# Optimization experiments

Measured on AMD Instinct MI355X. Metric: run time of the kernel, lower is better.

Reference implementation:

```python
import jax, jax.numpy as jnp
import numpy as np


def postorder_positions(depth):
    """Post-order index of each node in a perfect binary tree of given depth.
    Returns dict: level -> np.array of post-order indices for the left-to-right
    nodes at that level (level 0 = leaves, level `depth` = root)."""
    levels = {0: np.array([0], dtype=np.int64)}
    size = 1  # size of depth-(d-1) subtree
    for d in range(1, depth + 1):
        new = {l: np.concatenate([levels[l], levels[l] + size]) for l in range(d)}
        new[d] = np.array([2 * size], dtype=np.int64)
        levels = new
        size = 2 * size + 1
    return levels


def setup_inputs() -> dict:
    key = jax.random.key(0)
    k1, k2, k3, k4, k5, k6 = jax.random.split(key, 6)
    VOCAB, E, LBL, LEAVES = 50000, 100, 2, 131072  # 2**17 leaves
    word_ids = jax.random.randint(k1, (LEAVES,), 0, VOCAB, dtype=jnp.int32)
    emb_table = jax.random.normal(k2, (VOCAB, E), dtype=jnp.float32) * 0.1
    Wl = jax.random.normal(k3, (E, E), dtype=jnp.float32) * 0.1
    bl = jax.random.normal(k4, (E,), dtype=jnp.float32) * 0.1
    Wp = jax.random.normal(k5, (LBL, E), dtype=jnp.float32) * 0.1
    bp = jax.random.normal(k6, (LBL,), dtype=jnp.float32) * 0.1
    return {"word_ids": word_ids, "emb_table": emb_table, "Wl": Wl, "bl": bl, "Wp": Wp, "bp": bp}


def reference(word_ids, emb_table, Wl, bl, Wp, bp):
    # Perfect binary tree, batched level-by-level (same math as the per-node
    # Python recursion in the torch module). NOTE: original uses fcl for BOTH
    # children, so internal node = relu(fcl(left) + fcl(right)).
    L = word_ids.shape[0]
    D = int(round(np.log2(L)))
    pos = postorder_positions(D)
    n_nodes = 2 * L - 1

    h = emb_table[word_ids]  # [L, E] leaf states
    out = jnp.zeros((n_nodes, 1, bp.shape[0]), dtype=h.dtype)
    for lvl in range(D + 1):
        proj = h @ Wp.T + bp                     # [n_lvl, label]
        out = out.at[jnp.asarray(pos[lvl])].set(proj[:, None, :])
        if lvl < D:
            # fcl(left)+fcl(right) = (left+right) @ Wl^T + 2*bl, then relu
            h = jax.nn.relu((h[0::2] + h[1::2]) @ Wl.T + 2.0 * bl)
    return out  # [n_nodes, 1, label] in post-order, matching torch.cat(node_list)
```

## Files before the change

kernel.cpp:

```cpp
#include <hip/hip_runtime.h>

typedef _Float16 h8v __attribute__((ext_vector_type(8)));
typedef float f4v __attribute__((ext_vector_type(4)));

#define RS 136
#define SD 68

__device__ __forceinline__ unsigned pk2f(float a, float b) {
  unsigned short ha = __builtin_bit_cast(unsigned short, (_Float16)a);
  unsigned short hb = __builtin_bit_cast(unsigned short, (_Float16)b);
  return (unsigned)ha | ((unsigned)hb << 16);
}
__device__ __forceinline__ float2 upk(unsigned u) {
  _Float16 lo = __builtin_bit_cast(_Float16, (unsigned short)(u & 0xffffu));
  _Float16 hi = __builtin_bit_cast(_Float16, (unsigned short)(u >> 16));
  return make_float2((float)lo, (float)hi);
}

__global__ void prep_kernel(const float* __restrict__ Wl,
                            unsigned short* __restrict__ Wlf) {
  int i = blockIdx.x * 256 + threadIdx.x;
  if (i < 128 * 128) {
    int o = i >> 7, k = i & 127;
    _Float16 v = (_Float16)0.f;
    if (o < 100 && k < 100) v = (_Float16)Wl[o * 100 + k];
    Wlf[i] = __builtin_bit_cast(unsigned short, v);
  }
}

__device__ __forceinline__ void load_bfrags(
    const unsigned short* __restrict__ Wlf, const float* __restrict__ bl,
    h8v (&B0)[4], h8v (&B1)[4], float& bias0, float& bias1,
    int wave, int quad, int c16) {
  int col0 = wave * 32 + c16;
  int col1 = col0 + 16;
  bias0 = (col0 < 100) ? 2.0f * bl[col0] : 0.f;
  bias1 = (col1 < 100) ? 2.0f * bl[col1] : 0.f;
  const _Float16* w0 = (const _Float16*)Wlf + col0 * 128 + quad * 8;
  const _Float16* w1 = (const _Float16*)Wlf + col1 * 128 + quad * 8;
  B0[0] = *(const h8v*)(w0);      B0[1] = *(const h8v*)(w0 + 32);
  B0[2] = *(const h8v*)(w0 + 64); B0[3] = *(const h8v*)(w0 + 96);
  B1[0] = *(const h8v*)(w1);      B1[1] = *(const h8v*)(w1 + 32);
  B1[2] = *(const h8v*)(w1 + 64); B1[3] = *(const h8v*)(w1 + 96);
}

__device__ __forceinline__ void mfma_level(
    const _Float16* srcE, const _Float16* srcO, bool pairMode,
    _Float16* dstE, _Float16* dstO, int nOut,
    const h8v (&B0)[4], const h8v (&B1)[4], float bias0, float bias1,
    int lane, int wave) {
  const int quad = lane >> 4, c16 = lane & 15;
  const int col0 = wave * 32 + c16, col1 = col0 + 16;
  const int tiles = (nOut + 15) >> 4;
  for (int rt = 0; rt < tiles; ++rt) {
    const int r = rt * 16 + c16;
    const h8v* pe = (const h8v*)(srcE + (size_t)r * RS + quad * 8);
    h8v A0, A1, A2, A3;
    if (pairMode) {
      const h8v* po = (const h8v*)(srcO + (size_t)r * RS + quad * 8);
      A0 = pe[0] + po[0];  A1 = pe[4] + po[4];
      A2 = pe[8] + po[8];  A3 = pe[12] + po[12];
    } else {
      A0 = pe[0]; A1 = pe[4]; A2 = pe[8]; A3 = pe[12];
    }
    f4v a0 = {bias0, bias0, bias0, bias0};
    f4v a1 = {bias1, bias1, bias1, bias1};
    a0 = __builtin_amdgcn_mfma_f32_16x16x32_f16(A0, B0[0], a0, 0, 0, 0);
    a0 = __builtin_amdgcn_mfma_f32_16x16x32_f16(A1, B0[1], a0, 0, 0, 0);
    a0 = __builtin_amdgcn_mfma_f32_16x16x32_f16(A2, B0[2], a0, 0, 0, 0);
    a0 = __builtin_amdgcn_mfma_f32_16x16x32_f16(A3, B0[3], a0, 0, 0, 0);
    a1 = __builtin_amdgcn_mfma_f32_16x16x32_f16(A0, B1[0], a1, 0, 0, 0);
    a1 = __builtin_amdgcn_mfma_f32_16x16x32_f16(A1, B1[1], a1, 0, 0, 0);
    a1 = __builtin_amdgcn_mfma_f32_16x16x32_f16(A2, B1[2], a1, 0, 0, 0);
    a1 = __builtin_amdgcn_mfma_f32_16x16x32_f16(A3, B1[3], a1, 0, 0, 0);
    #pragma unroll
    for (int rg = 0; rg < 4; ++rg) {
      int row = rt * 16 + quad * 4 + rg;
      _Float16* dr = ((row & 1) ? dstO : dstE) + (size_t)(row >> 1) * RS;
      dr[col0] = (_Float16)fmaxf(a0[rg], 0.f);
      dr[col1] = (_Float16)fmaxf(a1[rg], 0.f);
    }
  }
}

__device__ __forceinline__ void proj_rows(
    const _Float16* E, const _Float16* O, int nRows, const float* WpS,
    float bp0, float bp1, int lvl, long gbase, float* __restrict__ out, int tid) {
  if (tid >= nRows) return;
  const unsigned* row = (const unsigned*)((tid & 1) ? O : E) + (size_t)(tid >> 1) * SD;
  float q0 = bp0, q1 = bp1;
  #pragma unroll
  for (int p = 0; p < 25; ++p) {
    uint2 u = ((const uint2*)row)[p];
    float2 a = upk(u.x), b = upk(u.y);
    q0 = fmaf(a.x, WpS[4*p], fmaf(a.y, WpS[4*p+1],
         fmaf(b.x, WpS[4*p+2], fmaf(b.y, WpS[4*p+3], q0))));
    q1 = fmaf(a.x, WpS[100+4*p], fmaf(a.y, WpS[100+4*p+1],
         fmaf(b.x, WpS[100+4*p+2], fmaf(b.y, WpS[100+4*p+3], q1))));
  }
  long g = gbase + tid;
  long pos = ((g + 1) << (lvl + 1)) - 2 - __popc((unsigned)g);
  out[2 * pos] = q0; out[2 * pos + 1] = q1;
}

__global__ __launch_bounds__(256, 3) void leaf_kernel(
    const int* __restrict__ word_ids, const float* __restrict__ emb,
    const unsigned short* __restrict__ Wlf, const float* __restrict__ bl,
    const float* __restrict__ Wp, const float* __restrict__ bp,
    unsigned* __restrict__ h7g, float* __restrict__ out) {
  __shared__ _Float16 S1[64 * RS];
  __shared__ _Float16 Ea[32 * RS], Oa[32 * RS];
  __shared__ _Float16 Eb[16 * RS], Ob[16 * RS];
  __shared__ float WpS[200];
  const int tid = threadIdx.x, lane = tid & 63;
  const int wave = __builtin_amdgcn_readfirstlane(tid >> 6);
  const int quad = lane >> 4, c16 = lane & 15;
  const int blk = blockIdx.x;

  if (tid < 200) WpS[tid] = Wp[tid];
  {
    unsigned* S1d = (unsigned*)S1;
    for (int i = tid; i < 64 * 14; i += 256) S1d[(i / 14) * SD + 50 + (i % 14)] = 0;
  }
  const float bp0 = bp[0], bp1 = bp[1];

  const int l = tid >> 1, hh = tid & 1;
  const long gL = (long)blk * 128 + l;
  const float4* row4 = (const float4*)(emb + (size_t)word_ids[gL] * 100);
  float4 v[13];
  #pragma unroll
  for (int i = 0; i < 13; ++i) {
    int q = 13 * hh + i;
    if (q < 25) v[i] = row4[q];
  }
  __syncthreads();

  {
    float q0 = 0.f, q1 = 0.f;
    #pragma unroll
    for (int i = 0; i < 13; ++i) {
      int q = 13 * hh + i;
      if (q < 25) {
        q0 = fmaf(v[i].x, WpS[4*q], fmaf(v[i].y, WpS[4*q+1],
             fmaf(v[i].z, WpS[4*q+2], fmaf(v[i].w, WpS[4*q+3], q0))));
        q1 = fmaf(v[i].x, WpS[100+4*q], fmaf(v[i].y, WpS[100+4*q+1],
             fmaf(v[i].z, WpS[100+4*q+2], fmaf(v[i].w, WpS[100+4*q+3], q1))));
      }
    }
    q0 += __shfl_xor(q0, 1, 64);
    q1 += __shfl_xor(q1, 1, 64);
    if (hh == 0) {
      long pos = ((gL + 1) << 1) - 2 - __popc((unsigned)gL);
      out[2 * pos] = q0 + bp0; out[2 * pos + 1] = q1 + bp1;
    }
  }
  {
    unsigned* S1d = (unsigned*)S1;
    #pragma unroll
    for (int i = 0; i < 13; ++i) {
      int q = 13 * hh + i;
      if (q < 25) {
        float sx = v[i].x + __shfl_xor(v[i].x, 2, 64);
        float sy = v[i].y + __shfl_xor(v[i].y, 2, 64);
        float sz = v[i].z + __shfl_xor(v[i].z, 2, 64);
        float sw = v[i].w + __shfl_xor(v[i].w, 2, 64);
        if ((tid & 2) == 0) {
          int m = tid >> 2;
          S1d[m * SD + 2*q]     = pk2f(sx, sy);
          S1d[m * SD + 2*q + 1] = pk2f(sz, sw);
        }
      }
    }
  }
  h8v B0[4], B1[4]; float bias0, bias1;
  load_bfrags(Wlf, bl, B0, B1, bias0, bias1, wave, quad, c16);
  __syncthreads();

  mfma_level(S1, nullptr, false, Ea, Oa, 64, B0, B1, bias0, bias1, lane, wave);
  __syncthreads();
  mfma_level(Ea, Oa, true, Eb, Ob, 32, B0, B1, bias0, bias1, lane, wave);
  proj_rows(Ea, Oa, 64, WpS, bp0, bp1, 1, (long)blk * 64, out, tid);
  __syncthreads();
  mfma_level(Eb, Ob, true, Ea, Oa, 16, B0, B1, bias0, bias1, lane, wave);
  proj_rows(Eb, Ob, 32, WpS, bp0, bp1, 2, (long)blk * 32, out, tid);
  __syncthreads();
  mfma_level(Ea, Oa, true, Eb, Ob, 8, B0, B1, bias0, bias1, lane, wave);
  proj_rows(Ea, Oa, 16, WpS, bp0, bp1, 3, (long)blk * 16, out, tid);
  __syncthreads();
  mfma_level(Eb, Ob, true, Ea, Oa, 4, B0, B1, bias0, bias1, lane, wave);
  proj_rows(Eb, Ob, 8, WpS, bp0, bp1, 4, (long)blk * 8, out, tid);
  __syncthreads();
  mfma_level(Ea, Oa, true, Eb, Ob, 2, B0, B1, bias0, bias1, lane, wave);
  proj_rows(Ea, Oa, 4, WpS, bp0, bp1, 5, (long)blk * 4, out, tid);
  __syncthreads();
  mfma_level(Eb, Ob, true, Ea, Oa, 1, B0, B1, bias0, bias1, lane, wave);
  proj_rows(Eb, Ob, 2, WpS, bp0, bp1, 6, (long)blk * 2, out, tid);
  __syncthreads();
  if (tid < 50) h7g[(size_t)blk * 50 + tid] = ((unsigned*)Ea)[tid];
}

__global__ __launch_bounds__(256) void tree_kernel(
    const unsigned* __restrict__ hsrc, unsigned* __restrict__ hdst,
    const unsigned short* __restrict__ Wlf, const float* __restrict__ bl,
    const float* __restrict__ Wp, const float* __restrict__ bp,
    float* __restrict__ out, int firstLvl, int nLvl, int nIn, int finalProj) {
  __shared__ _Float16 Ea[32 * RS], Oa[32 * RS];
  __shared__ _Float16 Eb[16 * RS], Ob[16 * RS];
  __shared__ float WpS[200];
  const int tid = threadIdx.x, lane = tid & 63;
  const int wave = __builtin_amdgcn_readfirstlane(tid >> 6);
  const int quad = lane >> 4, c16 = lane & 15;
  const int blk = blockIdx.x;

  if (tid < 200) WpS[tid] = Wp[tid];
  const float bp0 = bp[0], bp1 = bp[1];

  {
    const unsigned* src = hsrc + (size_t)blk * nIn * 50;
    unsigned* Ed = (unsigned*)Ea; unsigned* Od = (unsigned*)Oa;
    for (int i = tid; i < 64 * 64; i += 256) {
      int r = i >> 6, d = i & 63;
      unsigned val = (r < nIn && d < 50) ? src[(size_t)r * 50 + d] : 0u;
      ((r & 1) ? Od : Ed)[(r >> 1) * SD + d] = val;
    }
    unsigned* Ed2 = (unsigned*)Eb; unsigned* Od2 = (unsigned*)Ob;
    for (int i = tid; i < 32 * 64; i += 256) {
      int r = i >> 6, d = i & 63;
      ((r & 1) ? Od2 : Ed2)[(r >> 1) * SD + d] = 0u;
    }
  }
  h8v B0[4], B1[4]; float bias0, bias1;
  load_bfrags(Wlf, bl, B0, B1, bias0, bias1, wave, quad, c16);
  __syncthreads();

  _Float16 *sE = Ea, *sO = Oa, *dE = Eb, *dO = Ob;
  int n = nIn >> 1;
  for (int p = 0; p < nLvl; ++p) {
    mfma_level(sE, sO, true, dE, dO, n, B0, B1, bias0, bias1, lane, wave);
    proj_rows(sE, sO, n * 2, WpS, bp0, bp1, firstLvl + p - 1,
              (long)blk * (n * 2), out, tid);
    __syncthreads();
    _Float16* t;
    t = sE; sE = dE; dE = t;
    t = sO; sO = dO; dO = t;
    n >>= 1;
  }
  int R = nIn >> nLvl;
  if (finalProj)
    proj_rows(sE, sO, R, WpS, bp0, bp1, firstLvl + nLvl - 1, (long)blk * R, out, tid);
  if (hdst) {
    for (int i = tid; i < R * 50; i += 256) {
      int r = i / 50, d = i % 50;
      hdst[(size_t)blk * R * 50 + i] =
          ((const unsigned*)((r & 1) ? sO : sE))[(r >> 1) * SD + d];
    }
  }
}

extern "C" void kernel_launch(void* const* d_in, const int* in_sizes, int n_in,
                              void* d_out, int out_size, void* d_ws, size_t ws_size,
                              hipStream_t stream) {
  const int*   word_ids = (const int*)  d_in[0];
  const float* emb      = (const float*)d_in[1];
  const float* Wl       = (const float*)d_in[2];
  const float* bl       = (const float*)d_in[3];
  const float* Wp       = (const float*)d_in[4];
  const float* bp       = (const float*)d_in[5];
  float* out = (float*)d_out;

  unsigned short* Wlf = (unsigned short*)d_ws;
  unsigned* h7g  = (unsigned*)((char*)d_ws + 32768);
  unsigned* h13g = (unsigned*)((char*)d_ws + 32768 + 204800);

  prep_kernel<<<64, 256, 0, stream>>>(Wl, Wlf);
  leaf_kernel<<<1024, 256, 0, stream>>>(word_ids, emb, Wlf, bl, Wp, bp, h7g, out);
  tree_kernel<<<16, 256, 0, stream>>>(h7g, h13g, Wlf, bl, Wp, bp, out, 8, 6, 64, 0);
  tree_kernel<<<1, 256, 0, stream>>>(h13g, nullptr, Wlf, bl, Wp, bp, out, 14, 4, 16, 1);
}
```

Measured before the change: 152.2 us.

## Restructure tree into 512-thread leaf kernel and single tail kernel

The leaf kernel now runs 512 threads per block over 256 leaves, with waves split into column pairs and row halves, and reduces 8 levels in shared memory. The two small tree_kernel launches are replaced by one 512-thread tail kernel that reads the level-8 states from global memory and reduces the remaining levels. The aim is to cut a kernel launch and its serial dependency, and to use more waves on the tiny upper levels. The cost is larger shared memory per block (about 70KB for leaf, 100KB for tail), which lowers occupancy, and a single-block tail that serializes 9 levels.

Measured after the change: 152.3 us. About the same (+0.1%).

```diff
diff --git a/kernel.cpp b/kernel.cpp
--- a/kernel.cpp
+++ b/kernel.cpp
@@ -31,8 +31,8 @@
 __device__ __forceinline__ void load_bfrags(
     const unsigned short* __restrict__ Wlf, const float* __restrict__ bl,
     h8v (&B0)[4], h8v (&B1)[4], float& bias0, float& bias1,
-    int wave, int quad, int c16) {
-  int col0 = wave * 32 + c16;
+    int cp, int quad, int c16) {
+  int col0 = cp * 32 + c16;
   int col1 = col0 + 16;
   bias0 = (col0 < 100) ? 2.0f * bl[col0] : 0.f;
   bias1 = (col1 < 100) ? 2.0f * bl[col1] : 0.f;
@@ -44,15 +44,42 @@
   B1[2] = *(const h8v*)(w1 + 64); B1[3] = *(const h8v*)(w1 + 96);
 }
 
+__device__ __forceinline__ void mfma_8(
+    const h8v& A0, const h8v& A1, const h8v& A2, const h8v& A3,
+    const h8v (&B0)[4], const h8v (&B1)[4], float bias0, float bias1,
+    f4v& a0, f4v& a1) {
+  a0 = {bias0, bias0, bias0, bias0};
+  a1 = {bias1, bias1, bias1, bias1};
+  a0 = __builtin_amdgcn_mfma_f32_16x16x32_f16(A0, B0[0], a0, 0, 0, 0);
+  a0 = __builtin_amdgcn_mfma_f32_16x16x32_f16(A1, B0[1], a0, 0, 0, 0);
+  a0 = __builtin_amdgcn_mfma_f32_16x16x32_f16(A2, B0[2], a0, 0, 0, 0);
+  a0 = __builtin_amdgcn_mfma_f32_16x16x32_f16(A3, B0[3], a0, 0, 0, 0);
+  a1 = __builtin_amdgcn_mfma_f32_16x16x32_f16(A0, B1[0], a1, 0, 0, 0);
+  a1 = __builtin_amdgcn_mfma_f32_16x16x32_f16(A1, B1[1], a1, 0, 0, 0);
+  a1 = __builtin_amdgcn_mfma_f32_16x16x32_f16(A2, B1[2], a1, 0, 0, 0);
+  a1 = __builtin_amdgcn_mfma_f32_16x16x32_f16(A3, B1[3], a1, 0, 0, 0);
+}
+
+__device__ __forceinline__ void store_cd(
+    _Float16* dstE, _Float16* dstO, int rb, const f4v& a0, const f4v& a1,
+    int quad, int c16, int col0, int col1) {
+  #pragma unroll
+  for (int rg = 0; rg < 4; ++rg) {
+    int row = rb + quad * 4 + rg;
+    _Float16* dr = ((row & 1) ? dstO : dstE) + (size_t)(row >> 1) * RS;
+    dr[col0] = (_Float16)fmaxf(a0[rg], 0.f);
+    dr[col1] = (_Float16)fmaxf(a1[rg], 0.f);
+  }
+}
+
 __device__ __forceinline__ void mfma_level(
     const _Float16* srcE, const _Float16* srcO, bool pairMode,
     _Float16* dstE, _Float16* dstO, int nOut,
     const h8v (&B0)[4], const h8v (&B1)[4], float bias0, float bias1,
-    int lane, int wave) {
-  const int quad = lane >> 4, c16 = lane & 15;
-  const int col0 = wave * 32 + c16, col1 = col0 + 16;
+    int cp, int rowhalf, int quad, int c16) {
+  const int col0 = cp * 32 + c16, col1 = col0 + 16;
   const int tiles = (nOut + 15) >> 4;
-  for (int rt = 0; rt < tiles; ++rt) {
+  for (int rt = rowhalf; rt < tiles; rt += 2) {
     const int r = rt * 16 + c16;
     const h8v* pe = (const h8v*)(srcE + (size_t)r * RS + quad * 8);
     h8v A0, A1, A2, A3;
@@ -63,23 +90,28 @@
     } else {
       A0 = pe[0]; A1 = pe[4]; A2 = pe[8]; A3 = pe[12];
     }
-    f4v a0 = {bias0, bias0, bias0, bias0};
-    f4v a1 = {bias1, bias1, bias1, bias1};
-    a0 = __builtin_amdgcn_mfma_f32_16x16x32_f16(A0, B0[0], a0, 0, 0, 0);
-    a0 = __builtin_amdgcn_mfma_f32_16x16x32_f16(A1, B0[1], a0, 0, 0, 0);
-    a0 = __builtin_amdgcn_mfma_f32_16x16x32_f16(A2, B0[2], a0, 0, 0, 0);
-    a0 = __builtin_amdgcn_mfma_f32_16x16x32_f16(A3, B0[3], a0, 0, 0, 0);
-    a1 = __builtin_amdgcn_mfma_f32_16x16x32_f16(A0, B1[0], a1, 0, 0, 0);
-    a1 = __builtin_amdgcn_mfma_f32_16x16x32_f16(A1, B1[1], a1, 0, 0, 0);
-    a1 = __builtin_amdgcn_mfma_f32_16x16x32_f16(A2, B1[2], a1, 0, 0, 0);
-    a1 = __builtin_amdgcn_mfma_f32_16x16x32_f16(A3, B1[3], a1, 0, 0, 0);
-    #pragma unroll
-    for (int rg = 0; rg < 4; ++rg) {
-      int row = rt * 16 + quad * 4 + rg;
-      _Float16* dr = ((row & 1) ? dstO : dstE) + (size_t)(row >> 1) * RS;
-      dr[col0] = (_Float16)fmaxf(a0[rg], 0.f);
-      dr[col1] = (_Float16)fmaxf(a1[rg], 0.f);
-    }
+    f4v a0, a1;
+    mfma_8(A0, A1, A2, A3, B0, B1, bias0, bias1, a0, a1);
+    store_cd(dstE, dstO, rt * 16, a0, a1, quad, c16, col0, col1);
+  }
+}
+
+__device__ __forceinline__ void mfma_level_g(
+    const _Float16* __restrict__ g, _Float16* dstE, _Float16* dstO,
+    const h8v (&B0)[4], const h8v (&B1)[4], float bias0, float bias1,
+    int cp, int rowhalf, int quad, int c16) {
+  const int col0 = cp * 32 + c16, col1 = col0 + 16;
+  for (int rt = rowhalf; rt < 16; rt += 2) {
+    const int r = rt * 16 + c16;
+    const _Float16* g0 = g + (size_t)(2 * r) * 100 + quad * 8;
+    const _Float16* g1 = g0 + 100;
+    h8v A0 = *(const h8v*)(g0)      + *(const h8v*)(g1);
+    h8v A1 = *(const h8v*)(g0 + 32) + *(const h8v*)(g1 + 32);
+    h8v A2 = *(const h8v*)(g0 + 64) + *(const h8v*)(g1 + 64);
+    h8v A3 = *(const h8v*)(g0 + 96) + *(const h8v*)(g1 + 96);
+    f4v a0, a1;
+    mfma_8(A0, A1, A2, A3, B0, B1, bias0, bias1, a0, a1);
+    store_cd(dstE, dstO, rt * 16, a0, a1, quad, c16, col0, col1);
   }
 }
 
@@ -103,29 +135,29 @@
   out[2 * pos] = q0; out[2 * pos + 1] = q1;
 }
 
-__global__ __launch_bounds__(256, 3) void leaf_kernel(
+__global__ __launch_bounds__(512) void leaf_kernel(
     const int* __restrict__ word_ids, const float* __restrict__ emb,
     const unsigned short* __restrict__ Wlf, const float* __restrict__ bl,
     const float* __restrict__ Wp, const float* __restrict__ bp,
-    unsigned* __restrict__ h7g, float* __restrict__ out) {
-  __shared__ _Float16 S1[64 * RS];
-  __shared__ _Float16 Ea[32 * RS], Oa[32 * RS];
-  __shared__ _Float16 Eb[16 * RS], Ob[16 * RS];
+    unsigned* __restrict__ h8g, float* __restrict__ out) {
+  __shared__ __align__(16) _Float16 bufA[128 * RS];
+  __shared__ __align__(16) _Float16 bufB[128 * RS];
   __shared__ float WpS[200];
   const int tid = threadIdx.x, lane = tid & 63;
   const int wave = __builtin_amdgcn_readfirstlane(tid >> 6);
+  const int cp = wave >> 1, rowhalf = wave & 1;
   const int quad = lane >> 4, c16 = lane & 15;
   const int blk = blockIdx.x;
 
   if (tid < 200) WpS[tid] = Wp[tid];
   {
-    unsigned* S1d = (unsigned*)S1;
-    for (int i = tid; i < 64 * 14; i += 256) S1d[(i / 14) * SD + 50 + (i % 14)] = 0;
+    unsigned* Ad = (unsigned*)bufA;
+    for (int i = tid; i < 128 * 14; i += 512) Ad[(i / 14) * SD + 50 + (i % 14)] = 0;
   }
   const float bp0 = bp[0], bp1 = bp[1];
 
   const int l = tid >> 1, hh = tid & 1;
-  const long gL = (long)blk * 128 + l;
+  const long gL = (long)blk * 256 + l;
   const float4* row4 = (const float4*)(emb + (size_t)word_ids[gL] * 100);
   float4 v[13];
   #pragma unroll
@@ -155,7 +187,7 @@
     }
   }
   {
-    unsigned* S1d = (unsigned*)S1;
+    unsigned* Ad = (unsigned*)bufA;
     #pragma unroll
     for (int i = 0; i < 13; ++i) {
       int q = 13 * hh + i;
@@ -166,95 +198,89 @@
         float sw = v[i].w + __shfl_xor(v[i].w, 2, 64);
         if ((tid & 2) == 0) {
           int m = tid >> 2;
-          S1d[m * SD + 2*q]     = pk2f(sx, sy);
-          S1d[m * SD + 2*q + 1] = pk2f(sz, sw);
+          Ad[m * SD + 2*q]     = pk2f(sx, sy);
+          Ad[m * SD + 2*q + 1] = pk2f(sz, sw);
         }
       }
     }
   }
   h8v B0[4], B1[4]; float bias0, bias1;
-  load_bfrags(Wlf, bl, B0, B1, bias0, bias1, wave, quad, c16);
-  __syncthreads();
-
-  mfma_level(S1, nullptr, false, Ea, Oa, 64, B0, B1, bias0, bias1, lane, wave);
-  __syncthreads();
-  mfma_level(Ea, Oa, true, Eb, Ob, 32, B0, B1, bias0, bias1, lane, wave);
-  proj_rows(Ea, Oa, 64, WpS, bp0, bp1, 1, (long)blk * 64, out, tid);
-  __syncthreads();
-  mfma_level(Eb, Ob, true, Ea, Oa, 16, B0, B1, bias0, bias1, lane, wave);
-  proj_rows(Eb, Ob, 32, WpS, bp0, bp1, 2, (long)blk * 32, out, tid);
-  __syncthreads();
-  mfma_level(Ea, Oa, true, Eb, Ob, 8, B0, B1, bias0, bias1, lane, wave);
-  proj_rows(Ea, Oa, 16, WpS, bp0, bp1, 3, (long)blk * 16, out, tid);
-  __syncthreads();
-  mfma_level(Eb, Ob, true, Ea, Oa, 4, B0, B1, bias0, bias1, lane, wave);
-  proj_rows(Eb, Ob, 8, WpS, bp0, bp1, 4, (long)blk * 8, out, tid);
-  __syncthreads();
-  mfma_level(Ea, Oa, true, Eb, Ob, 2, B0, B1, bias0, bias1, lane, wave);
-  proj_rows(Ea, Oa, 4, WpS, bp0, bp1, 5, (long)blk * 4, out, tid);
-  __syncthreads();
-  mfma_level(Eb, Ob, true, Ea, Oa, 1, B0, B1, bias0, bias1, lane, wave);
-  proj_rows(Eb, Ob, 2, WpS, bp0, bp1, 6, (long)blk * 2, out, tid);
-  __syncthreads();
-  if (tid < 50) h7g[(size_t)blk * 50 + tid] = ((unsigned*)Ea)[tid];
-}
-
-__global__ __launch_bounds__(256) void tree_kernel(
-    const unsigned* __restrict__ hsrc, unsigned* __restrict__ hdst,
-    const unsigned short* __restrict__ Wlf, const float* __restrict__ bl,
-    const float* __restrict__ Wp, const float* __restrict__ bp,
-    float* __restrict__ out, int firstLvl, int nLvl, int nIn, int finalProj) {
-  __shared__ _Float16 Ea[32 * RS], Oa[32 * RS];
-  __shared__ _Float16 Eb[16 * RS], Ob[16 * RS];
+  load_bfrags(Wlf, bl, B0, B1, bias0, bias1, cp, quad, c16);
+  __syncthreads();
+
+  mfma_level(bufA, nullptr, false, bufB, bufB + 64 * RS, 128,
+             B0, B1, bias0, bias1, cp, rowhalf, quad, c16);
+  __syncthreads();
+
+  const _Float16 *sE = bufB, *sO = bufB + 64 * RS;
+  int n = 64;
+  #pragma unroll 1
+  for (int j = 0; j < 7; ++j) {
+    _Float16* d = (j & 1) ? bufB : bufA;
+    int oOff = (n >> 1) > 8 ? (n >> 1) : 8;
+    mfma_level(sE, sO, true, d, d + (size_t)oOff * RS, n,
+               B0, B1, bias0, bias1, cp, rowhalf, quad, c16);
+    proj_rows(sE, sO, n * 2, WpS, bp0, bp1, j + 1, (long)blk * (n * 2), out, tid);
+    __syncthreads();
+    sE = d; sO = d + (size_t)oOff * RS;
+    n >>= 1;
+  }
+  if (tid < 50) h8g[(size_t)blk * 50 + tid] = ((const unsigned*)sE)[tid];
+}
+
+__global__ __launch_bounds__(512) void tail_kernel(
+    const _Float16* __restrict__ h8g, const unsigned short* __restrict__ Wlf,
+    const float* __restrict__ bl, const float* __restrict__ Wp,
+    const float* __restrict__ bp, float* __restrict__ out) {
+  __shared__ __align__(16) _Float16 bufA[256 * RS];
+  __shared__ __align__(16) _Float16 bufB[128 * RS];
   __shared__ float WpS[200];
   const int tid = threadIdx.x, lane = tid & 63;
   const int wave = __builtin_amdgcn_readfirstlane(tid >> 6);
+  const int cp = wave >> 1, rowhalf = wave & 1;
   const int quad = lane >> 4, c16 = lane & 15;
-  const int blk = blockIdx.x;
 
   if (tid < 200) WpS[tid] = Wp[tid];
+  h8v B0[4], B1[4]; float bias0, bias1;
+  load_bfrags(Wlf, bl, B0, B1, bias0, bias1, cp, quad, c16);
+  __syncthreads();
   const float bp0 = bp[0], bp1 = bp[1];
 
   {
-    const unsigned* src = hsrc + (size_t)blk * nIn * 50;
-    unsigned* Ed = (unsigned*)Ea; unsigned* Od = (unsigned*)Oa;
-    for (int i = tid; i < 64 * 64; i += 256) {
-      int r = i >> 6, d = i & 63;
-      unsigned val = (r < nIn && d < 50) ? src[(size_t)r * 50 + d] : 0u;
-      ((r & 1) ? Od : Ed)[(r >> 1) * SD + d] = val;
-    }
-    unsigned* Ed2 = (unsigned*)Eb; unsigned* Od2 = (unsigned*)Ob;
-    for (int i = tid; i < 32 * 64; i += 256) {
-      int r = i >> 6, d = i & 63;
-      ((r & 1) ? Od2 : Ed2)[(r >> 1) * SD + d] = 0u;
-    }
-  }
-  h8v B0[4], B1[4]; float bias0, bias1;
-  load_bfrags(Wlf, bl, B0, B1, bias0, bias1, wave, quad, c16);
-  __syncthreads();
-
-  _Float16 *sE = Ea, *sO = Oa, *dE = Eb, *dO = Ob;
-  int n = nIn >> 1;
-  for (int p = 0; p < nLvl; ++p) {
-    mfma_level(sE, sO, true, dE, dO, n, B0, B1, bias0, bias1, lane, wave);
-    proj_rows(sE, sO, n * 2, WpS, bp0, bp1, firstLvl + p - 1,
-              (long)blk * (n * 2), out, tid);
+    const unsigned* row = (const unsigned*)h8g + (size_t)tid * 50;
+    float q0 = bp0, q1 = bp1;
+    #pragma unroll
+    for (int p = 0; p < 25; ++p) {
+      uint2 u = ((const uint2*)row)[p];
+      float2 a = upk(u.x), b = upk(u.y);
+      q0 = fmaf(a.x, WpS[4*p], fmaf(a.y, WpS[4*p+1],
+           fmaf(b.x, WpS[4*p+2], fmaf(b.y, WpS[4*p+3], q0))));
+      q1 = fmaf(a.x, WpS[100+4*p], fmaf(a.y, WpS[100+4*p+1],
+           fmaf(b.x, WpS[100+4*p+2], fmaf(b.y, WpS[100+4*p+3], q1))));
+    }
+    long g = tid;
+    long pos = ((g + 1) << 9) - 2 - __popc((unsigned)g);
+    out[2 * pos] = q0; out[2 * pos + 1] = q1;
+  }
+
+  mfma_level_g(h8g, bufA, bufA + 128 * RS, B0, B1, bias0, bias1,
+               cp, rowhalf, quad, c16);
+  __syncthreads();
+
+  const _Float16 *sE = bufA, *sO = bufA + 128 * RS;
+  int n = 128;
+  #pragma unroll 1
+  for (int j = 0; j < 8; ++j) {
+    _Float16* d = (j & 1) ? bufA : bufB;
+    int oOff = (n >> 1) > 8 ? (n >> 1) : 8;
+    mfma_level(sE, sO, true, d, d + (size_t)oOff * RS, n,
+               B0, B1, bias0, bias1, cp, rowhalf, quad, c16);
+    proj_rows(sE, sO, n * 2, WpS, bp0, bp1, 9 + j, 0, out, tid);
     __syncthreads();
-    _Float16* t;
-    t = sE; sE = dE; dE = t;
-    t = sO; sO = dO; dO = t;
+    sE = d; sO = d + (size_t)oOff * RS;
     n >>= 1;
   }
-  int R = nIn >> nLvl;
-  if (finalProj)
-    proj_rows(sE, sO, R, WpS, bp0, bp1, firstLvl + nLvl - 1, (long)blk * R, out, tid);
-  if (hdst) {
-    for (int i = tid; i < R * 50; i += 256) {
-      int r = i / 50, d = i % 50;
-      hdst[(size_t)blk * R * 50 + i] =
-          ((const unsigned*)((r & 1) ? sO : sE))[(r >> 1) * SD + d];
-    }
-  }
+  proj_rows(sE, sO, 1, WpS, bp0, bp1, 17, 0, out, tid);
 }
 
 extern "C" void kernel_launch(void* const* d_in, const int* in_sizes, int n_in,
@@ -269,11 +295,9 @@
   float* out = (float*)d_out;
 
   unsigned short* Wlf = (unsigned short*)d_ws;
-  unsigned* h7g  = (unsigned*)((char*)d_ws + 32768);
-  unsigned* h13g = (unsigned*)((char*)d_ws + 32768 + 204800);
+  unsigned* h8g = (unsigned*)((char*)d_ws + 32768);
 
   prep_kernel<<<64, 256, 0, stream>>>(Wl, Wlf);
-  leaf_kernel<<<1024, 256, 0, stream>>>(word_ids, emb, Wlf, bl, Wp, bp, h7g, out);
-  tree_kernel<<<16, 256, 0, stream>>>(h7g, h13g, Wlf, bl, Wp, bp, out, 8, 6, 64, 0);
-  tree_kernel<<<1, 256, 0, stream>>>(h13g, nullptr, Wlf, bl, Wp, bp, out, 14, 4, 16, 1);
-}
+  leaf_kernel<<<512, 512, 0, stream>>>(word_ids, emb, Wlf, bl, Wp, bp, h8g, out);
+  tail_kernel<<<1, 512, 0, stream>>>((const _Float16*)h8g, Wlf, bl, Wp, bp, out);
+}
```
